# Kernel tuning notes

Hardware: AMD Instinct MI355X
Metric: run time of the kernel (lower is better)

Reference implementation:

```python
import jax, jax.numpy as jnp
import numpy as np

B, C, N, T = 8, 64, 128, 288
PRED_LEN, CYCLE_LEN, SHORT_P, KSZ = 12, 24, 12, 2
SEQ_LEN = T
EPS = 0.01


def _const_extrap(x, p):
    # replicate-pad last value p times on the right
    return jnp.pad(x, ((0, 0), (0, 0), (0, 0), (0, p)), mode='edge')


def _period_norm(x, p):
    # sliding-window mean/var of width p (window ends at each position),
    # left replicate-padded to full length -- same math as torch stack+mean
    zshape = x.shape[:-1] + (1,)
    cs = jnp.concatenate([jnp.zeros(zshape, x.dtype), jnp.cumsum(x, axis=-1)], axis=-1)
    cs2 = jnp.concatenate([jnp.zeros(zshape, x.dtype), jnp.cumsum(x * x, axis=-1)], axis=-1)
    mean = (cs[..., p:] - cs[..., :-p]) / p                      # (b,c,n,t-p+1)
    var = (cs2[..., p:] - cs2[..., :-p]) / p - mean ** 2 + 1e-5
    pad = ((0, 0), (0, 0), (0, 0), (p - 1, 0))
    mean = jnp.pad(mean, pad, mode='edge')
    var = jnp.pad(var, pad, mode='edge')
    out = (x - mean) / jnp.sqrt(var + EPS)
    return out, mean, jnp.sqrt(var)


def _seasonal_norm(x, p):
    b, c, n, t = x.shape
    k = t // p
    xp = x.reshape(b, c, n, k, p)                                # chunks of length p
    mean = xp.mean(axis=3)                                       # (b,c,n,p)
    var = (xp * xp).mean(axis=3) - mean ** 2 + 1e-5
    mean = jnp.tile(mean, (1, 1, 1, k))
    var = jnp.tile(var, (1, 1, 1, k))
    r = t % p  # circular left-pad (0 for our config)
    if r:
        mean = jnp.concatenate([mean[..., -r:], mean], axis=-1)
        var = jnp.concatenate([var[..., -r:], var], axis=-1)
    out = (x - mean) / jnp.sqrt(var + EPS)
    return out, mean, jnp.sqrt(var)


def _seasonal_extrap(x, cl, pl, cn):
    b, c, n, t = x.shape
    # torch builds softmax(zeros) -> uniform mixing weights (a constant)
    w = jax.nn.softmax(jnp.zeros((pl // cl + 1, cn), x.dtype), axis=-1)
    xc = x.reshape(b, c, n, cn, cl).transpose(0, 1, 2, 4, 3)     # (b,c,n,cl,cn)
    proj = jnp.einsum('pk,bcnlk->bcnlp', w, xc)                  # (b,c,n,cl,P+1)
    full = jnp.concatenate([xc, proj], axis=-1)                  # (b,c,n,cl,cn+P+1)
    return full.transpose(0, 1, 2, 4, 3).reshape(b, c, n, -1)[..., :t + pl]


def _spatial_norm(x, emb):
    n = emb.shape[0]
    adj = jax.nn.softmax(emb @ emb.T - 10.0 * jnp.eye(n, dtype=emb.dtype), axis=-1)
    mean = jnp.einsum('nm,bcmt->bcnt', adj, x)
    var = jnp.einsum('nm,bcmt->bcnt', adj, x * x) - mean ** 2 + 1e-5
    out = (x - mean) / jnp.sqrt(var + EPS)
    return out, mean, jnp.sqrt(var)


def _residual_extrap(x, w, bias, in_len, pl):
    # conv2d kernel (1, in_len) over last in_len steps -> (b, c*pl, n, 1)
    b, c, n, t = x.shape
    proj = jnp.einsum('bcnl,ocl->bon', x[..., -in_len:], w[:, :, 0, :]) + bias[None, :, None]
    proj = proj.reshape(b, pl, c, n).transpose(0, 2, 3, 1)       # torch reshape(b,-1,c,n).permute
    return jnp.concatenate([x, proj], axis=-1)


def _conv_k(x, w, bias):
    out = jax.lax.conv_general_dilated(x, w, (1, 1), 'VALID',
                                       dimension_numbers=('NCHW', 'OIHW', 'NCHW'))
    return out + bias[None, :, None, None]


def _conv1x1(x, w, bias):
    return jnp.einsum('oc,bcnt->bont', w[:, :, 0, 0], x) + bias[None, :, None, None]


def _forward(x, node_emb, re1_w, re1_b, re2_w, re2_b, re3_w, re3_b, re4_w, re4_b,
             conv1_w, conv1_b, conv2_w, conv2_b, skip_w, skip_b, res_w, res_b):
    xs = [_const_extrap(x, PRED_LEN)]
    x, lt_mean, lt_std = _period_norm(x, SEQ_LEN)
    xs += [_residual_extrap(x, re1_w, re1_b, SHORT_P, PRED_LEN),
           _const_extrap(lt_mean, PRED_LEN), _const_extrap(lt_std, PRED_LEN)]
    x, s_mean, s_std = _seasonal_norm(x, CYCLE_LEN)
    cn = SEQ_LEN // CYCLE_LEN
    xs += [_residual_extrap(x, re2_w, re2_b, SHORT_P, PRED_LEN),
           _seasonal_extrap(s_mean, CYCLE_LEN, PRED_LEN, cn),
           _seasonal_extrap(s_std, CYCLE_LEN, PRED_LEN, cn)]
    x, st_mean, st_std = _period_norm(x, SHORT_P)
    xs += [_residual_extrap(x, re3_w, re3_b, SHORT_P, PRED_LEN),
           _const_extrap(st_mean, PRED_LEN), _const_extrap(st_std, PRED_LEN)]
    x, sp_mean, sp_std = _spatial_norm(x, node_emb)
    xs += [_residual_extrap(x, re4_w, re4_b, SHORT_P, PRED_LEN),
           _const_extrap(sp_mean, PRED_LEN), _const_extrap(sp_std, PRED_LEN)]
    xcat = jnp.concatenate(xs, axis=1)                           # (b, 13c, n, t+pred)
    xcat = jnp.pad(xcat, ((0, 0), (0, 0), (0, 0), (KSZ - 1, 0)))  # causal zero pad
    z = jnp.tanh(_conv_k(xcat, conv1_w, conv1_b)) * jax.nn.sigmoid(_conv_k(xcat, conv2_w, conv2_b))
    x_z = _conv1x1(z[..., :-PRED_LEN], res_w, res_b)
    s = _conv1x1(z[..., -PRED_LEN:], skip_w, skip_b)
    return (x_z, s)


def setup_inputs() -> dict:
    key = jax.random.key(0)
    ks = jax.random.split(key, 12)
    d = {"x": jax.random.normal(ks[0], (B, C, N, T), jnp.float32)}
    d["node_emb"] = 0.1 * jax.random.normal(ks[1], (N, C), jnp.float32)
    for i, nm in enumerate(["re1", "re2", "re3", "re4"]):
        d[nm + "_w"] = 0.02 * jax.random.normal(ks[2 + i], (C * PRED_LEN, C, 1, SHORT_P), jnp.float32)
        d[nm + "_b"] = jnp.zeros((C * PRED_LEN,), jnp.float32)
    d["conv1_w"] = 0.02 * jax.random.normal(ks[6], (C, 13 * C, 1, KSZ), jnp.float32)
    d["conv1_b"] = jnp.zeros((C,), jnp.float32)
    d["conv2_w"] = 0.02 * jax.random.normal(ks[7], (C, 13 * C, 1, KSZ), jnp.float32)
    d["conv2_b"] = jnp.zeros((C,), jnp.float32)
    d["skip_w"] = 0.05 * jax.random.normal(ks[8], (C, C, 1, 1), jnp.float32)
    d["skip_b"] = jnp.zeros((C,), jnp.float32)
    d["res_w"] = 0.05 * jax.random.normal(ks[9], (C, C, 1, 1), jnp.float32)
    d["res_b"] = jnp.zeros((C,), jnp.float32)
    return d


def reference(x, node_emb, re1_w, re1_b, re2_w, re2_b, re3_w, re3_b, re4_w, re4_b,
              conv1_w, conv1_b, conv2_w, conv2_b, skip_w, skip_b, res_w, res_b):
    return _forward(x, node_emb, re1_w, re1_b, re2_w, re2_b, re3_w, re3_b, re4_w, re4_b,
                    conv1_w, conv1_b, conv2_w, conv2_b, skip_w, skip_b, res_w, res_b)
```

## Files before the change

### kernel.cpp

```cpp
#include <hip/hip_runtime.h>
#include <math.h>

typedef unsigned short u16;
typedef unsigned int u32;
typedef __attribute__((ext_vector_type(8))) short s8v;
typedef __attribute__((ext_vector_type(4))) float f4v;

#define Bx 8
#define Cx 64
#define Nx 128
#define Tx 288
#define PL 12
#define CL 24
#define SP 12
#define TOUT 300
#define EPSV 0.01f
#define NTb 2359296L

__device__ __forceinline__ float b2f(u16 h) {
  union { u32 u; float f; } v; v.u = ((u32)h) << 16; return v.f;
}
__device__ __forceinline__ u16 f2b(float f) {
  union { float f; u32 u; } v; v.f = f;
  return (u16)((v.u + 0x7FFFu + ((v.u >> 16) & 1u)) >> 16);
}

__global__ __launch_bounds__(64) void k0_adj(const float* __restrict__ emb,
                                             float* __restrict__ adjT) {
  int n = blockIdx.x;
  int lane = threadIdx.x;
  float d0 = 0.f, d1 = 0.f;
  for (int k = 0; k < 64; ++k) {
    float e = emb[n * 64 + k];
    d0 += e * emb[lane * 64 + k];
    d1 += e * emb[(lane + 64) * 64 + k];
  }
  if (lane == n) d0 -= 10.f;
  if (lane + 64 == n) d1 -= 10.f;
  float mx = fmaxf(d0, d1);
  for (int off = 32; off; off >>= 1) mx = fmaxf(mx, __shfl_xor(mx, off, 64));
  float e0 = expf(d0 - mx), e1 = expf(d1 - mx);
  float sm = e0 + e1;
  for (int off = 32; off; off >>= 1) sm += __shfl_xor(sm, off, 64);
  float inv = 1.f / sm;
  adjT[lane * 128 + n] = e0 * inv;
  adjT[(lane + 64) * 128 + n] = e1 * inv;
}

__global__ __launch_bounds__(256) void k_wprep(
    const float* __restrict__ cw1, const float* __restrict__ cw2,
    const float* __restrict__ rsw, const float* __restrict__ skw,
    u16* __restrict__ W16, u16* __restrict__ WR16, u16* __restrict__ WS16) {
  int R = blockIdx.x;
  const float* src = (R < 64) ? (cw1 + (long)R * 1664) : (cw2 + (long)(R - 64) * 1664);
  for (int k = threadIdx.x; k < 1664; k += 256) {
    int j = k >> 7;
    int rem = k & 127;
    int tap = rem >> 6, cc = rem & 63;
    int kc = rem >> 5;
    W16[(j * 4 + kc) * 4096 + R * 32 + (rem & 31)] = f2b(src[(j * 64 + cc) * 2 + tap]);
  }
  if (R < 64) {
    for (int k = threadIdx.x; k < 64; k += 256) {
      int h = k >> 5;
      WR16[(h * 64 + R) * 32 + (k & 31)] = f2b(rsw[R * 64 + k]);
      WS16[(h * 64 + R) * 32 + (k & 31)] = f2b(skw[R * 64 + k]);
    }
  }
}

__global__ __launch_bounds__(256) void k_wprep2(
    const float* __restrict__ w0, const float* __restrict__ w1,
    const float* __restrict__ w2, const float* __restrict__ w3,
    u16* __restrict__ WJ16) {
  int idx0 = blockIdx.x * 256 + threadIdx.x;
  for (int idx = idx0; idx < 2359296; idx += 256 * 256) {
    int j = idx / 589824;
    int r = idx - j * 589824;
    const float* w = (j == 0) ? w0 : (j == 1) ? w1 : (j == 2) ? w2 : w3;
    WJ16[idx] = f2b(w[r]);
  }
}

__global__ __launch_bounds__(256) void k1_chain(
    const float* __restrict__ xb, float* __restrict__ ltm, float* __restrict__ lts,
    float* __restrict__ pm, float* __restrict__ ps, u16* __restrict__ stm,
    u16* __restrict__ sts, u16* __restrict__ x3, u16* __restrict__ SG) {
  __shared__ float lds[4 * 352];
  int tid = threadIdx.x;
  int wv = tid >> 6, lane = tid & 63;
  float* buf = lds + wv * 352;
  float* pat = buf + 288;
  long s = (long)blockIdx.x * 4 + wv;
  const float* xs = xb + s * Tx;

  int b_loc = (int)(s >> 13);
  int cin = ((int)s >> 7) & 63;
  int n = (int)s & 127;
  long sg0 = (((long)b_loc * 4) * 128 + n) * 768 + cin * 12;

  float v[5];
  float sum = 0.f, sum2 = 0.f;
#pragma unroll
  for (int i = 0; i < 5; ++i) {
    int t = lane + 64 * i;
    if (t < Tx) { v[i] = xs[t]; sum += v[i]; sum2 += v[i] * v[i]; }
    else v[i] = 0.f;
  }
  for (int off = 32; off; off >>= 1) {
    sum += __shfl_xor(sum, off, 64);
    sum2 += __shfl_xor(sum2, off, 64);
  }
  float mean = sum * (1.f / 288.f);
  float var = sum2 * (1.f / 288.f) - mean * mean + 1e-5f;
  float sd = sqrtf(var);
  float r1 = rsqrtf(var + EPSV);
  if (lane == 0) { ltm[s] = mean; lts[s] = sd; }
#pragma unroll
  for (int i = 0; i < 5; ++i) {
    int t = lane + 64 * i;
    if (t < Tx) {
      float x1v = (v[i] - mean) * r1;
      v[i] = x1v;
      buf[t] = x1v;
      if (t >= Tx - SP) SG[sg0 + t - (Tx - SP)] = f2b(x1v);
    }
  }
  __syncthreads();
  if (lane < CL) {
    float a = 0.f, b2 = 0.f;
    for (int k = 0; k < 12; ++k) {
      float u = buf[k * CL + lane];
      a += u; b2 += u * u;
    }
    float pmv = a * (1.f / 12.f);
    float pvar = b2 * (1.f / 12.f) - pmv * pmv + 1e-5f;
    float psd = sqrtf(pvar);
    pat[lane] = pmv; pat[CL + lane] = psd;
    pm[s * CL + lane] = pmv; ps[s * CL + lane] = psd;
  }
  __syncthreads();
  float w2v[5];
#pragma unroll
  for (int i = 0; i < 5; ++i) {
    int t = lane + 64 * i;
    if (t < Tx) {
      int l = t % CL;
      float pmv = pat[l], psd = pat[CL + l];
      float x2v = (v[i] - pmv) * rsqrtf(psd * psd + EPSV);
      w2v[i] = x2v;
      if (t >= Tx - SP) SG[sg0 + 98304 + t - (Tx - SP)] = f2b(x2v);
    } else w2v[i] = 0.f;
  }
  __syncthreads();
#pragma unroll
  for (int i = 0; i < 5; ++i) {
    int t = lane + 64 * i;
    if (t < Tx) buf[t] = w2v[i];
  }
  __syncthreads();
#pragma unroll
  for (int i = 0; i < 5; ++i) {
    int t = lane + 64 * i;
    if (t < Tx) {
      int te = t < 11 ? 11 : t;
      float a = 0.f, b2 = 0.f;
#pragma unroll
      for (int jj = 0; jj < 12; ++jj) {
        float u = buf[te - 11 + jj];
        a += u; b2 += u * u;
      }
      float m = a * (1.f / 12.f);
      float varw = b2 * (1.f / 12.f) - m * m + 1e-5f;
      stm[s * Tx + t] = f2b(m);
      sts[s * Tx + t] = f2b(sqrtf(varw));
      u16 xb3 = f2b((w2v[i] - m) * rsqrtf(varw + EPSV));
      x3[s * Tx + t] = xb3;
      if (t >= Tx - SP) SG[sg0 + 2 * 98304 + t - (Tx - SP)] = xb3;
    }
  }
}

__global__ __launch_bounds__(128) void k2_spatial(
    const u16* __restrict__ x3, const float* __restrict__ adjT,
    u16* __restrict__ x4, u16* __restrict__ spm, u16* __restrict__ sps,
    u16* __restrict__ SG) {
  __shared__ float X[128 * 36];
  int bid = blockIdx.x;
  int tc = bid % 9;
  long c = bid / 9;
  int t0 = tc * 32;
  int tid = threadIdx.x;
  for (int idx = tid; idx < 128 * 32; idx += 128) {
    int m = idx >> 5, i = idx & 31;
    X[m * 36 + i] = b2f(x3[(c * 128 + m) * Tx + t0 + i]);
  }
  __syncthreads();
  float a1[32], a2[32];
#pragma unroll
  for (int i = 0; i < 32; ++i) { a1[i] = 0.f; a2[i] = 0.f; }
  for (int m = 0; m < 128; ++m) {
    float a = adjT[m * 128 + tid];
    const float4* xp = (const float4*)&X[m * 36];
#pragma unroll
    for (int ii = 0; ii < 8; ++ii) {
      float4 xq = xp[ii];
      float t0v = a * xq.x; a1[ii * 4 + 0] += t0v; a2[ii * 4 + 0] += t0v * xq.x;
      float t1v = a * xq.y; a1[ii * 4 + 1] += t1v; a2[ii * 4 + 1] += t1v * xq.y;
      float t2v = a * xq.z; a1[ii * 4 + 2] += t2v; a2[ii * 4 + 2] += t2v * xq.z;
      float t3v = a * xq.w; a1[ii * 4 + 3] += t3v; a2[ii * 4 + 3] += t3v * xq.w;
    }
  }
  long sOut = c * 128 + tid;
  u32 xw[16], mw[16], sw[16];
#pragma unroll
  for (int p = 0; p < 16; ++p) {
    u32 xl = 0, ml = 0, sl = 0;
#pragma unroll
    for (int h = 0; h < 2; ++h) {
      int i = p * 2 + h;
      float mean = a1[i];
      float varv = a2[i] - mean * mean + 1e-5f;
      float xv = X[tid * 36 + i];
      xl |= ((u32)f2b((xv - mean) * rsqrtf(varv + EPSV))) << (16 * h);
      ml |= ((u32)f2b(mean)) << (16 * h);
      sl |= ((u32)f2b(sqrtf(varv))) << (16 * h);
    }
    xw[p] = xl; mw[p] = ml; sw[p] = sl;
  }
  long base = sOut * Tx + t0;
  uint4* xd = (uint4*)(x4 + base);
  uint4* md = (uint4*)(spm + base);
  uint4* sd = (uint4*)(sps + base);
#pragma unroll
  for (int k = 0; k < 4; ++k) {
    uint4 a, b, d;
    a.x = xw[k * 4]; a.y = xw[k * 4 + 1]; a.z = xw[k * 4 + 2]; a.w = xw[k * 4 + 3];
    b.x = mw[k * 4]; b.y = mw[k * 4 + 1]; b.z = mw[k * 4 + 2]; b.w = mw[k * 4 + 3];
    d.x = sw[k * 4]; d.y = sw[k * 4 + 1]; d.z = sw[k * 4 + 2]; d.w = sw[k * 4 + 3];
    xd[k] = a; md[k] = b; sd[k] = d;
  }
  if (tc == 8) {
    long sg = (((c >> 6) * 4 + 3) * 128 + tid) * 768 + (long)(c & 63) * 12;
    u32* sp = (u32*)(SG + sg);
#pragma unroll
    for (int k = 0; k < 6; ++k) sp[k] = xw[10 + k];
  }
}

__global__ __launch_bounds__(256) void k3_mfma(
    const u16* __restrict__ SG, const u16* __restrict__ WJ16,
    const float* __restrict__ bb0, const float* __restrict__ bb1,
    const float* __restrict__ bb2, const float* __restrict__ bb3,
    u16* __restrict__ tails) {
  __shared__ u16 Al[64 * 40];
  __shared__ u16 Bl[128 * 40];
  int bid = blockIdx.x;
  int ot = bid % 6;
  int rest = bid / 6;
  int nt = rest & 1;
  int bj = rest >> 1;
  int j = bj & 3;
  int tid = threadIdx.x;
  int wv = tid >> 6, lane = tid & 63;
  int wo = wv & 1, wm = wv >> 1;
  int rlane = lane & 15, glane = lane >> 4;
  int klane = glane * 8;

  const float* Bv = (j == 0) ? bb0 : (j == 1) ? bb1 : (j == 2) ? bb2 : bb3;
  const u16* Abase = SG + (long)bj * 98304 + (long)(nt * 64) * 768;
  const u16* Wbase = WJ16 + (long)j * 589824 + (long)(ot * 128) * 768;

  f4v acc[2][4];
#pragma unroll
  for (int ct = 0; ct < 4; ++ct) {
    float bvv = Bv[ot * 128 + wo * 64 + ct * 16 + rlane];
#pragma unroll
    for (int rt = 0; rt < 2; ++rt)
#pragma unroll
      for (int reg = 0; reg < 4; ++reg) acc[rt][ct][reg] = bvv;
  }

  int srow = tid >> 2, sseg = tid & 3;
  for (int ks = 0; ks < 24; ++ks) {
    int q0 = ks * 32;
    __syncthreads();
    *(float4*)(Al + srow * 40 + sseg * 8) =
        *(const float4*)(Abase + (long)srow * 768 + q0 + sseg * 8);
    *(float4*)(Bl + srow * 40 + sseg * 8) =
        *(const float4*)(Wbase + (long)srow * 768 + q0 + sseg * 8);
    *(float4*)(Bl + (srow + 64) * 40 + sseg * 8) =
        *(const float4*)(Wbase + (long)(srow + 64) * 768 + q0 + sseg * 8);
    __syncthreads();
    s8v av[2], bv[4];
#pragma unroll
    for (int rt = 0; rt < 2; ++rt)
      av[rt] = *(const s8v*)(Al + (wm * 32 + rt * 16 + rlane) * 40 + klane);
#pragma unroll
    for (int ct = 0; ct < 4; ++ct)
      bv[ct] = *(const s8v*)(Bl + (wo * 64 + ct * 16 + rlane) * 40 + klane);
#pragma unroll
    for (int rt = 0; rt < 2; ++rt)
#pragma unroll
      for (int ct = 0; ct < 4; ++ct)
        acc[rt][ct] = __builtin_amdgcn_mfma_f32_16x16x32_bf16(av[rt], bv[ct], acc[rt][ct], 0, 0, 0);
  }

  long outbase = (long)bj * 98304;
#pragma unroll
  for (int rt = 0; rt < 2; ++rt) {
    int nn = nt * 64 + wm * 32 + rt * 16 + glane * 4;
#pragma unroll
    for (int ct = 0; ct < 4; ++ct) {
      int o = ot * 128 + wo * 64 + ct * 16 + rlane;
#pragma unroll
      for (int reg = 0; reg < 4; ++reg)
        tails[outbase + (long)(nn + reg) * 768 + o] = f2b(acc[rt][ct][reg]);
    }
  }
}

template<int MODE>
__device__ __forceinline__ void stage_one(
    u16* __restrict__ Bb, const u16* __restrict__ T,
    const float* __restrict__ Tf, const float* __restrict__ fm,
    const float* __restrict__ fs, const float* __restrict__ fpm,
    const float* __restrict__ fps, const u16* __restrict__ tl,
    int n, int t0, int ccp, int u) {
  int cc0 = ccp * 2;
  int tg = t0 - 1 + u;
  u32 w = 0;
  if (MODE == 0) {
    if ((unsigned)tg < (unsigned)TOUT) {
      int tcl = tg < Tx ? tg : Tx - 1;
      const u16* p = T + ((long)cc0 * 128 + n) * Tx + tcl;
      w = (u32)p[0] | ((u32)p[128 * Tx] << 16);
    }
  } else if (MODE == 1) {
    if ((unsigned)tg < (unsigned)Tx) {
      const u16* p = T + ((long)cc0 * 128 + n) * Tx + tg;
      w = (u32)p[0] | ((u32)p[128 * Tx] << 16);
    } else if (tg >= Tx && tg < TOUT) {
      w = *(const u32*)(tl + (long)n * 768 + (tg - Tx) * 64 + cc0);
    }
  } else if (MODE == 2) {
    if ((unsigned)tg < (unsigned)TOUT)
      w = (u32)f2b(Tf[cc0 * 128 + n]) | ((u32)f2b(Tf[(cc0 + 1) * 128 + n]) << 16);
  } else if (MODE == 3) {
    if ((unsigned)tg < (unsigned)TOUT) {
      int l = tg % CL;
      w = (u32)f2b(Tf[((long)cc0 * 128 + n) * CL + l]) |
          ((u32)f2b(Tf[((long)(cc0 + 1) * 128 + n) * CL + l]) << 16);
    }
  } else if (MODE == 4) {
    if ((unsigned)tg < (unsigned)TOUT) {
      int tcl = tg < Tx ? tg : Tx - 1;
      const float* p = Tf + ((long)cc0 * 128 + n) * Tx + tcl;
      w = (u32)f2b(p[0]) | ((u32)f2b(p[128 * Tx]) << 16);
    }
  } else if (MODE == 5) {
    if ((unsigned)tg < (unsigned)Tx) {
      long s0 = (long)cc0 * 128 + n, s1 = s0 + 128;
      float v0 = (Tf[s0 * Tx + tg] - fm[s0]) * rsqrtf(fs[s0] * fs[s0] + EPSV);
      float v1 = (Tf[s1 * Tx + tg] - fm[s1]) * rsqrtf(fs[s1] * fs[s1] + EPSV);
      w = (u32)f2b(v0) | ((u32)f2b(v1) << 16);
    } else if (tg >= Tx && tg < TOUT) {
      w = *(const u32*)(tl + (long)n * 768 + (tg - Tx) * 64 + cc0);
    }
  } else {
    if ((unsigned)tg < (unsigned)Tx) {
      long s0 = (long)cc0 * 128 + n, s1 = s0 + 128;
      int l = tg % CL;
      float x10 = (Tf[s0 * Tx + tg] - fm[s0]) * rsqrtf(fs[s0] * fs[s0] + EPSV);
      float x11 = (Tf[s1 * Tx + tg] - fm[s1]) * rsqrtf(fs[s1] * fs[s1] + EPSV);
      float p0 = fpm[s0 * CL + l], q0 = fps[s0 * CL + l];
      float p1 = fpm[s1 * CL + l], q1 = fps[s1 * CL + l];
      float v0 = (x10 - p0) * rsqrtf(q0 * q0 + EPSV);
      float v1 = (x11 - p1) * rsqrtf(q1 * q1 + EPSV);
      w = (u32)f2b(v0) | ((u32)f2b(v1) << 16);
    } else if (tg >= Tx && tg < TOUT) {
      w = *(const u32*)(tl + (long)n * 768 + (tg - Tx) * 64 + cc0);
    }
  }
  *(u32*)(Bb + u * 72 + cc0) = w;
}

template<int MODE>
__device__ __forceinline__ void stage_j(
    u16* __restrict__ Bb, const u16* __restrict__ T,
    const float* __restrict__ Tf, const float* __restrict__ fm,
    const float* __restrict__ fs, const float* __restrict__ fpm,
    const float* __restrict__ fps, const u16* __restrict__ tl,
    int n, int t0, int tid) {
#pragma unroll 1
  for (int idx = tid; idx < 1056; idx += 256) {
    int ccp = idx / 33;
    int u = idx - ccp * 33;
    stage_one<MODE>(Bb, T, Tf, fm, fs, fpm, fps, tl, n, t0, ccp, u);
  }
}

__global__ __launch_bounds__(256) void k4_mfma(
    const float* __restrict__ xbG, const float* __restrict__ ltmG,
    const float* __restrict__ ltsG, const float* __restrict__ pmG,
    const float* __restrict__ psG, const u16* __restrict__ stmG,
    const u16* __restrict__ stsG, const u16* __restrict__ x3G,
    const u16* __restrict__ x4G, const u16* __restrict__ spmG,
    const u16* __restrict__ spsG, const u16* __restrict__ tailsG,
    const u16* __restrict__ W16, const u16* __restrict__ WR16,
    const u16* __restrict__ WS16, const float* __restrict__ cb1,
    const float* __restrict__ cb2, const float* __restrict__ rsb,
    const float* __restrict__ skb,
    float* __restrict__ outXZG, float* __restrict__ outSG) {
  __shared__ __align__(16) unsigned char smemraw[9504];
  u16* Bs0 = (u16*)smemraw;
  u16* Bs1 = (u16*)(smemraw + 4752);
  u16* abuf = (u16*)smemraw;
  u16* zB = (u16*)(smemraw + 4608);

  int bid = blockIdx.x;
  int n = bid & 127;
  int q = bid >> 7;
  int b_loc = q / 10;
  int chunk = q - b_loc * 10;
  int t0 = chunk * 32;
  int tid = threadIdx.x;
  int wv = tid >> 6, lane = tid & 63;
  int rlane = lane & 15, glane = lane >> 4;
  int klane = glane * 8;

  const float* xb  = xbG + b_loc * NTb;
  const float* ltm = ltmG + (long)b_loc * 8192;
  const float* lts = ltsG + (long)b_loc * 8192;
  const float* pm  = pmG + (long)b_loc * 196608;
  const float* ps  = psG + (long)b_loc * 196608;
  const u16* stm = stmG + b_loc * NTb;
  const u16* sts = stsG + b_loc * NTb;
  const u16* x3  = x3G + b_loc * NTb;
  const u16* x4  = x4G + b_loc * NTb;
  const u16* spm = spmG + b_loc * NTb;
  const u16* sps = spsG + b_loc * NTb;
  const u16* tails = tailsG + (long)b_loc * 393216;
  float* outXZ = outXZG + b_loc * NTb;
  float* outS  = outSG + (long)b_loc * 8192 * PL;

  f4v acc[2][2];
#pragma unroll
  for (int rt = 0; rt < 2; ++rt) {
    int Rb = wv * 32 + rt * 16 + glane * 4;
#pragma unroll
    for (int reg = 0; reg < 4; ++reg) {
      int R = Rb + reg;
      float bv = (R < 64) ? cb1[R] : cb2[R - 64];
#pragma unroll
      for (int ct = 0; ct < 2; ++ct) acc[rt][ct][reg] = bv;
    }
  }

  u16* bs = Bs0;
  u16* bo = Bs1;
  stage_j<4>(bs, (const u16*)0, xb, 0, 0, 0, 0, (const u16*)0, n, t0, tid);

  for (int j = 0; j < 13; ++j) {
    __syncthreads();
    switch (j + 1) {
      case 1:  stage_j<5>(bo, 0, xb, ltm, lts, 0, 0, tails, n, t0, tid); break;
      case 2:  stage_j<2>(bo, 0, ltm, 0, 0, 0, 0, 0, n, t0, tid); break;
      case 3:  stage_j<2>(bo, 0, lts, 0, 0, 0, 0, 0, n, t0, tid); break;
      case 4:  stage_j<6>(bo, 0, xb, ltm, lts, pm, ps, tails + 98304, n, t0, tid); break;
      case 5:  stage_j<3>(bo, 0, pm, 0, 0, 0, 0, 0, n, t0, tid); break;
      case 6:  stage_j<3>(bo, 0, ps, 0, 0, 0, 0, 0, n, t0, tid); break;
      case 7:  stage_j<1>(bo, x3, 0, 0, 0, 0, 0, tails + 2 * 98304, n, t0, tid); break;
      case 8:  stage_j<0>(bo, stm, 0, 0, 0, 0, 0, 0, n, t0, tid); break;
      case 9:  stage_j<0>(bo, sts, 0, 0, 0, 0, 0, 0, n, t0, tid); break;
      case 10: stage_j<1>(bo, x4, 0, 0, 0, 0, 0, tails + 3 * 98304, n, t0, tid); break;
      case 11: stage_j<0>(bo, spm, 0, 0, 0, 0, 0, 0, n, t0, tid); break;
      case 12: stage_j<0>(bo, sps, 0, 0, 0, 0, 0, 0, n, t0, tid); break;
      default: break;
    }
#pragma unroll
    for (int kc = 0; kc < 4; ++kc) {
      const u16* wj = W16 + (j * 4 + kc) * 4096;
      s8v av[2], bv[2];
#pragma unroll
      for (int rt = 0; rt < 2; ++rt) {
        int R = wv * 32 + rt * 16 + rlane;
        av[rt] = *(const s8v*)(wj + R * 32 + klane);
      }
#pragma unroll
      for (int ct = 0; ct < 2; ++ct) {
        int row = ct * 16 + rlane + (kc >> 1);
        bv[ct] = *(const s8v*)(bs + row * 72 + (kc & 1) * 32 + klane);
      }
#pragma unroll
      for (int rt = 0; rt < 2; ++rt)
#pragma unroll
        for (int ct = 0; ct < 2; ++ct)
          acc[rt][ct] = __builtin_amdgcn_mfma_f32_16x16x32_bf16(av[rt], bv[ct], acc[rt][ct], 0, 0, 0);
    }
    u16* tsw = bs; bs = bo; bo = tsw;
  }

  __syncthreads();
  if (wv >= 2) {
#pragma unroll
    for (int rt = 0; rt < 2; ++rt)
#pragma unroll
      for (int ct = 0; ct < 2; ++ct)
#pragma unroll
        for (int reg = 0; reg < 4; ++reg) {
          int r = (wv - 2) * 32 + rt * 16 + glane * 4 + reg;
          int tl2 = ct * 16 + rlane;
          abuf[r * 36 + tl2] = f2b(acc[rt][ct][reg]);
        }
  }
  __syncthreads();
  if (wv < 2) {
#pragma unroll
    for (int rt = 0; rt < 2; ++rt)
#pragma unroll
      for (int ct = 0; ct < 2; ++ct)
#pragma unroll
        for (int reg = 0; reg < 4; ++reg) {
          int r = wv * 32 + rt * 16 + glane * 4 + reg;
          int tl2 = ct * 16 + rlane;
          float a2v = b2f(abuf[r * 36 + tl2]);
          float z = tanhf(acc[rt][ct][reg]) * (1.f / (1.f + expf(-a2v)));
          zB[tl2 * 72 + r] = f2b(z);
        }
  }
  __syncthreads();
  {
    int oL = wv * 16 + rlane;
    int oS = wv * 16 + glane * 4;
    s8v aR0 = *(const s8v*)(WR16 + oL * 32 + klane);
    s8v aR1 = *(const s8v*)(WR16 + 2048 + oL * 32 + klane);
    s8v aS0 = *(const s8v*)(WS16 + oL * 32 + klane);
    s8v aS1 = *(const s8v*)(WS16 + 2048 + oL * 32 + klane);
    for (int tt = 0; tt < 2; ++tt) {
      int tstart = t0 + tt * 16;
      if (tstart >= TOUT) break;
      bool res = tstart < Tx;
      s8v b0 = *(const s8v*)(zB + (tt * 16 + rlane) * 72 + klane);
      s8v b1 = *(const s8v*)(zB + (tt * 16 + rlane) * 72 + 32 + klane);
      f4v oa;
#pragma unroll
      for (int reg = 0; reg < 4; ++reg)
        oa[reg] = res ? rsb[oS + reg] : skb[oS + reg];
      if (res) {
        oa = __builtin_amdgcn_mfma_f32_16x16x32_bf16(aR0, b0, oa, 0, 0, 0);
        oa = __builtin_amdgcn_mfma_f32_16x16x32_bf16(aR1, b1, oa, 0, 0, 0);
        int tglob = tstart + rlane;
#pragma unroll
        for (int reg = 0; reg < 4; ++reg)
          outXZ[((long)(oS + reg) * 128 + n) * Tx + tglob] = oa[reg];
      } else {
        oa = __builtin_amdgcn_mfma_f32_16x16x32_bf16(aS0, b0, oa, 0, 0, 0);
        oa = __builtin_amdgcn_mfma_f32_16x16x32_bf16(aS1, b1, oa, 0, 0, 0);
        int tglob = tstart + rlane;
        if (tglob < TOUT) {
#pragma unroll
          for (int reg = 0; reg < 4; ++reg)
            outS[((long)(oS + reg) * 128 + n) * PL + (tglob - Tx)] = oa[reg];
        }
      }
    }
  }
}

extern "C" void kernel_launch(void* const* d_in, const int* in_sizes, int n_in,
                              void* d_out, int out_size, void* d_ws, size_t ws_size,
                              hipStream_t stream) {
  const float* x   = (const float*)d_in[0];
  const float* emb = (const float*)d_in[1];
  const float* rew[4] = {(const float*)d_in[2], (const float*)d_in[4],
                         (const float*)d_in[6], (const float*)d_in[8]};
  const float* reb[4] = {(const float*)d_in[3], (const float*)d_in[5],
                         (const float*)d_in[7], (const float*)d_in[9]};
  const float* c1w = (const float*)d_in[10];
  const float* c1b = (const float*)d_in[11];
  const float* c2w = (const float*)d_in[12];
  const float* c2b = (const float*)d_in[13];
  const float* skw = (const float*)d_in[14];
  const float* skb = (const float*)d_in[15];
  const float* rsw = (const float*)d_in[16];
  const float* rsb = (const float*)d_in[17];
  float* out = (float*)d_out;

  const size_t shared_bytes = 65536 + (52 * 4096 + 2 * 4096) * 2 + 2359296UL * 2;
  const size_t per_batch = 409600UL * 4 + (786432UL + 6UL * 2359296UL) * 2;
  int g = 1;
  if (shared_bytes + 8 * per_batch + 4096 <= ws_size) g = 8;
  else if (shared_bytes + 4 * per_batch + 4096 <= ws_size) g = 4;
  else if (shared_bytes + 2 * per_batch + 4096 <= ws_size) g = 2;

  float* ws = (float*)d_ws;
  float* adjT = ws;
  u16* W16  = (u16*)(adjT + 16384);
  u16* WR16 = W16 + 52 * 4096;
  u16* WS16 = WR16 + 4096;
  u16* WJ16 = WS16 + 4096;
  float* fbase = (float*)(WJ16 + 2359296);
  float* ltm = fbase;
  float* lts = ltm + (long)g * 8192;
  float* pmv = lts + (long)g * 8192;
  float* psv = pmv + (long)g * 196608;
  u16* tails16 = (u16*)(psv + (long)g * 196608);
  u16* SGb = tails16 + (long)g * 393216;
  u16* stm = SGb + (long)g * 393216;
  u16* sts = stm + (long)g * NTb;
  u16* x3  = sts + (long)g * NTb;
  u16* x4  = x3 + (long)g * NTb;
  u16* spm = x4 + (long)g * NTb;
  u16* sps = spm + (long)g * NTb;

  hipLaunchKernelGGL(k0_adj, dim3(128), dim3(64), 0, stream, emb, adjT);
  hipLaunchKernelGGL(k_wprep, dim3(128), dim3(256), 0, stream,
                     c1w, c2w, rsw, skw, W16, WR16, WS16);
  hipLaunchKernelGGL(k_wprep2, dim3(256), dim3(256), 0, stream,
                     rew[0], rew[1], rew[2], rew[3], WJ16);
  int ng = 8 / g;
  for (int gi = 0; gi < ng; ++gi) {
    long base = (long)gi * g;
    const float* xg = x + base * NTb;
    float* oXZ = out + base * NTb;
    float* oS  = out + (long)Bx * NTb + base * 8192 * PL;
    hipLaunchKernelGGL(k1_chain, dim3(g * 2048), dim3(256), 0, stream,
                       xg, ltm, lts, pmv, psv, stm, sts, x3, SGb);
    hipLaunchKernelGGL(k2_spatial, dim3(g * 576), dim3(128), 0, stream,
                       x3, adjT, x4, spm, sps, SGb);
    hipLaunchKernelGGL(k3_mfma, dim3(g * 48), dim3(256), 0, stream,
                       SGb, WJ16, reb[0], reb[1], reb[2], reb[3], tails16);
    hipLaunchKernelGGL(k4_mfma, dim3(g * 1280), dim3(256), 0, stream,
                       xg, ltm, lts, pmv, psv, stm, sts, x3, x4, spm, sps,
                       tails16, W16, WR16, WS16, c1b, c2b, rsb, skb, oXZ, oS);
  }
}
```

Before: 904.7 us.

## Compute spatial norm adjacency products with bf16 MFMA instead of scalar FMA

The spatial normalization kernel now computes the adjacency-weighted mean and second moment as two bf16 MFMA matrix products (adj·x and adj·x²), replacing the per-thread scalar FMA loop over 128 nodes. The adjacency matrix is stored as row-major bf16, and x² is precomputed in bf16 into shared memory. Outputs are staged through shared memory so global stores are coalesced. This cuts the FP32 ALU cost of the spatial stage, but rounding x² and adj to bf16 lowers precision of the variance and could hurt accuracy.

Measured after the change: 744.2 us. -17.7%, faster.

```diff
diff --git a/kernel.cpp b/kernel.cpp
--- a/kernel.cpp
+++ b/kernel.cpp
@@ -26,7 +26,7 @@
 }
 
 __global__ __launch_bounds__(64) void k0_adj(const float* __restrict__ emb,
-                                             float* __restrict__ adjT) {
+                                             u16* __restrict__ adjB) {
   int n = blockIdx.x;
   int lane = threadIdx.x;
   float d0 = 0.f, d1 = 0.f;
@@ -43,8 +43,8 @@
   float sm = e0 + e1;
   for (int off = 32; off; off >>= 1) sm += __shfl_xor(sm, off, 64);
   float inv = 1.f / sm;
-  adjT[lane * 128 + n] = e0 * inv;
-  adjT[(lane + 64) * 128 + n] = e1 * inv;
+  adjB[n * 128 + lane] = f2b(e0 * inv);
+  adjB[n * 128 + lane + 64] = f2b(e1 * inv);
 }
 
 __global__ __launch_bounds__(256) void k_wprep(
@@ -181,70 +181,118 @@
   }
 }
 
-__global__ __launch_bounds__(128) void k2_spatial(
-    const u16* __restrict__ x3, const float* __restrict__ adjT,
+__global__ __launch_bounds__(256) void k2_spatial(
+    const u16* __restrict__ x3, const u16* __restrict__ adjB,
     u16* __restrict__ x4, u16* __restrict__ spm, u16* __restrict__ sps,
     u16* __restrict__ SG) {
-  __shared__ float X[128 * 36];
+  __shared__ __align__(16) unsigned char sraw[48128];
+  u16* Xt = (u16*)sraw;
+  u16* Qt = (u16*)(sraw + 8704);
+  u16* oX = (u16*)(sraw + 17408);
+  u16* oM = (u16*)(sraw + 27648);
+  u16* oS = (u16*)(sraw + 37888);
   int bid = blockIdx.x;
   int tc = bid % 9;
   long c = bid / 9;
   int t0 = tc * 32;
   int tid = threadIdx.x;
-  for (int idx = tid; idx < 128 * 32; idx += 128) {
-    int m = idx >> 5, i = idx & 31;
-    X[m * 36 + i] = b2f(x3[(c * 128 + m) * Tx + t0 + i]);
-  }
-  __syncthreads();
-  float a1[32], a2[32];
-#pragma unroll
-  for (int i = 0; i < 32; ++i) { a1[i] = 0.f; a2[i] = 0.f; }
-  for (int m = 0; m < 128; ++m) {
-    float a = adjT[m * 128 + tid];
-    const float4* xp = (const float4*)&X[m * 36];
-#pragma unroll
-    for (int ii = 0; ii < 8; ++ii) {
-      float4 xq = xp[ii];
-      float t0v = a * xq.x; a1[ii * 4 + 0] += t0v; a2[ii * 4 + 0] += t0v * xq.x;
-      float t1v = a * xq.y; a1[ii * 4 + 1] += t1v; a2[ii * 4 + 1] += t1v * xq.y;
-      float t2v = a * xq.z; a1[ii * 4 + 2] += t2v; a2[ii * 4 + 2] += t2v * xq.z;
-      float t3v = a * xq.w; a1[ii * 4 + 3] += t3v; a2[ii * 4 + 3] += t3v * xq.w;
-    }
-  }
-  long sOut = c * 128 + tid;
-  u32 xw[16], mw[16], sw[16];
-#pragma unroll
-  for (int p = 0; p < 16; ++p) {
-    u32 xl = 0, ml = 0, sl = 0;
-#pragma unroll
-    for (int h = 0; h < 2; ++h) {
-      int i = p * 2 + h;
-      float mean = a1[i];
-      float varv = a2[i] - mean * mean + 1e-5f;
-      float xv = X[tid * 36 + i];
-      xl |= ((u32)f2b((xv - mean) * rsqrtf(varv + EPSV))) << (16 * h);
-      ml |= ((u32)f2b(mean)) << (16 * h);
-      sl |= ((u32)f2b(sqrtf(varv))) << (16 * h);
-    }
-    xw[p] = xl; mw[p] = ml; sw[p] = sl;
-  }
-  long base = sOut * Tx + t0;
-  uint4* xd = (uint4*)(x4 + base);
-  uint4* md = (uint4*)(spm + base);
-  uint4* sd = (uint4*)(sps + base);
-#pragma unroll
-  for (int k = 0; k < 4; ++k) {
-    uint4 a, b, d;
-    a.x = xw[k * 4]; a.y = xw[k * 4 + 1]; a.z = xw[k * 4 + 2]; a.w = xw[k * 4 + 3];
-    b.x = mw[k * 4]; b.y = mw[k * 4 + 1]; b.z = mw[k * 4 + 2]; b.w = mw[k * 4 + 3];
-    d.x = sw[k * 4]; d.y = sw[k * 4 + 1]; d.z = sw[k * 4 + 2]; d.w = sw[k * 4 + 3];
-    xd[k] = a; md[k] = b; sd[k] = d;
-  }
-  if (tc == 8) {
-    long sg = (((c >> 6) * 4 + 3) * 128 + tid) * 768 + (long)(c & 63) * 12;
-    u32* sp = (u32*)(SG + sg);
-#pragma unroll
-    for (int k = 0; k < 6; ++k) sp[k] = xw[10 + k];
+  int wv = tid >> 6, lane = tid & 63;
+  int rlane = lane & 15, glane = lane >> 4;
+  int klane = glane * 8;
+
+  {
+    int mp = tid & 63, tq = tid >> 6;
+    const u16* p0 = x3 + (c * 128 + 2 * mp) * Tx + t0 + 8 * tq;
+    uint4 a = *(const uint4*)p0;
+    uint4 b = *(const uint4*)(p0 + Tx);
+    u32 aw[4] = {a.x, a.y, a.z, a.w};
+    u32 bw[4] = {b.x, b.y, b.z, b.w};
+#pragma unroll
+    for (int q = 0; q < 4; ++q) {
+#pragma unroll
+      for (int h = 0; h < 2; ++h) {
+        int t = 8 * tq + q * 2 + h;
+        u16 lo = (u16)(aw[q] >> (16 * h));
+        u16 hi = (u16)(bw[q] >> (16 * h));
+        *(u32*)(Xt + t * 136 + 2 * mp) = (u32)lo | ((u32)hi << 16);
+        float fl = b2f(lo), fh = b2f(hi);
+        *(u32*)(Qt + t * 136 + 2 * mp) = (u32)f2b(fl * fl) | ((u32)f2b(fh * fh) << 16);
+      }
+    }
+  }
+  __syncthreads();
+
+  f4v am[2][2], aq[2][2];
+#pragma unroll
+  for (int rt = 0; rt < 2; ++rt)
+#pragma unroll
+    for (int ct = 0; ct < 2; ++ct) {
+#pragma unroll
+      for (int reg = 0; reg < 4; ++reg) { am[rt][ct][reg] = 0.f; aq[rt][ct][reg] = 0.f; }
+    }
+#pragma unroll
+  for (int kc = 0; kc < 4; ++kc) {
+    s8v av[2], bx[2], bq[2];
+#pragma unroll
+    for (int rt = 0; rt < 2; ++rt) {
+      int R = wv * 32 + rt * 16 + rlane;
+      av[rt] = *(const s8v*)(adjB + R * 128 + kc * 32 + klane);
+    }
+#pragma unroll
+    for (int ct = 0; ct < 2; ++ct) {
+      int tl = ct * 16 + rlane;
+      bx[ct] = *(const s8v*)(Xt + tl * 136 + kc * 32 + klane);
+      bq[ct] = *(const s8v*)(Qt + tl * 136 + kc * 32 + klane);
+    }
+#pragma unroll
+    for (int rt = 0; rt < 2; ++rt)
+#pragma unroll
+      for (int ct = 0; ct < 2; ++ct) {
+        am[rt][ct] = __builtin_amdgcn_mfma_f32_16x16x32_bf16(av[rt], bx[ct], am[rt][ct], 0, 0, 0);
+        aq[rt][ct] = __builtin_amdgcn_mfma_f32_16x16x32_bf16(av[rt], bq[ct], aq[rt][ct], 0, 0, 0);
+      }
+  }
+
+#pragma unroll
+  for (int rt = 0; rt < 2; ++rt)
+#pragma unroll
+    for (int ct = 0; ct < 2; ++ct) {
+      int tl = ct * 16 + rlane;
+#pragma unroll
+      for (int reg = 0; reg < 4; ++reg) {
+        int n = wv * 32 + rt * 16 + glane * 4 + reg;
+        float mean = am[rt][ct][reg];
+        float varv = aq[rt][ct][reg] - mean * mean + 1e-5f;
+        float xv = b2f(Xt[tl * 136 + n]);
+        oX[n * 40 + tl] = f2b((xv - mean) * rsqrtf(varv + EPSV));
+        oM[n * 40 + tl] = f2b(mean);
+        oS[n * 40 + tl] = f2b(sqrtf(varv));
+      }
+    }
+  __syncthreads();
+
+  {
+    int n2 = tid >> 1, half = tid & 1;
+    long basei = (c * 128 + n2) * Tx + t0 + half * 16;
+    uint4 v0 = *(const uint4*)(oX + n2 * 40 + half * 16);
+    uint4 v1 = *(const uint4*)(oX + n2 * 40 + half * 16 + 8);
+    *(uint4*)(x4 + basei) = v0;
+    *(uint4*)(x4 + basei + 8) = v1;
+    v0 = *(const uint4*)(oM + n2 * 40 + half * 16);
+    v1 = *(const uint4*)(oM + n2 * 40 + half * 16 + 8);
+    *(uint4*)(spm + basei) = v0;
+    *(uint4*)(spm + basei + 8) = v1;
+    v0 = *(const uint4*)(oS + n2 * 40 + half * 16);
+    v1 = *(const uint4*)(oS + n2 * 40 + half * 16 + 8);
+    *(uint4*)(sps + basei) = v0;
+    *(uint4*)(sps + basei + 8) = v1;
+    if (tc == 8 && half == 1) {
+      long sg = (((c >> 6) * 4 + 3) * 128 + n2) * 768 + (long)(c & 63) * 12;
+      u32* sp = (u32*)(SG + sg);
+      const u32* src = (const u32*)(oX + n2 * 40 + 20);
+#pragma unroll
+      for (int k = 0; k < 6; ++k) sp[k] = src[k];
+    }
   }
 }
 
@@ -595,8 +643,8 @@
   else if (shared_bytes + 2 * per_batch + 4096 <= ws_size) g = 2;
 
   float* ws = (float*)d_ws;
-  float* adjT = ws;
-  u16* W16  = (u16*)(adjT + 16384);
+  u16* adjB = (u16*)ws;
+  u16* W16  = (u16*)(ws + 16384);
   u16* WR16 = W16 + 52 * 4096;
   u16* WS16 = WR16 + 4096;
   u16* WJ16 = WS16 + 4096;
@@ -614,7 +662,7 @@
   u16* spm = x4 + (long)g * NTb;
   u16* sps = spm + (long)g * NTb;
 
-  hipLaunchKernelGGL(k0_adj, dim3(128), dim3(64), 0, stream, emb, adjT);
+  hipLaunchKernelGGL(k0_adj, dim3(128), dim3(64), 0, stream, emb, adjB);
   hipLaunchKernelGGL(k_wprep, dim3(128), dim3(256), 0, stream,
                      c1w, c2w, rsw, skw, W16, WR16, WS16);
   hipLaunchKernelGGL(k_wprep2, dim3(256), dim3(256), 0, stream,
@@ -627,8 +675,8 @@
     float* oS  = out + (long)Bx * NTb + base * 8192 * PL;
     hipLaunchKernelGGL(k1_chain, dim3(g * 2048), dim3(256), 0, stream,
                        xg, ltm, lts, pmv, psv, stm, sts, x3, SGb);
-    hipLaunchKernelGGL(k2_spatial, dim3(g * 576), dim3(128), 0, stream,
-                       x3, adjT, x4, spm, sps, SGb);
+    hipLaunchKernelGGL(k2_spatial, dim3(g * 576), dim3(256), 0, stream,
+                       x3, adjB, x4, spm, sps, SGb);
     hipLaunchKernelGGL(k3_mfma, dim3(g * 48), dim3(256), 0, stream,
                        SGb, WJ16, reb[0], reb[1], reb[2], reb[3], tails16);
     hipLaunchKernelGGL(k4_mfma, dim3(g * 1280), dim3(256), 0, stream,
```
